# Optimization experiments

Measured on AMD Instinct MI355X. Metric: run time of the kernel, lower is better.

## Reference

```python
import jax, jax.numpy as jnp
import numpy as np


def setup_inputs() -> dict:
    key = jax.random.key(0)
    ks = jax.random.split(key, 7)
    B, H, W, C = 8, 64, 64, 8
    d = C // 8  # q/k/v channels (= 1 here; forced by the module's broadcast-add)
    x = jax.random.normal(ks[0], (B, H, W, C), dtype=jnp.float32)
    # 1x1 convs == per-pixel linear layers: weight (C, d), bias (d,)
    scale = 1.0 / np.sqrt(C)
    Wq = jax.random.normal(ks[1], (C, d), dtype=jnp.float32) * scale
    bq = jnp.zeros((d,), dtype=jnp.float32)
    Wk = jax.random.normal(ks[2], (C, d), dtype=jnp.float32) * scale
    bk = jnp.zeros((d,), dtype=jnp.float32)
    Wv = jax.random.normal(ks[3], (C, d), dtype=jnp.float32) * scale
    bv = jnp.zeros((d,), dtype=jnp.float32)
    gamma = jnp.float32(0.5)  # nonzero so the attention branch matters
    return {"x": x, "Wq": Wq, "bq": bq, "Wk": Wk, "bk": bk, "Wv": Wv, "bv": bv, "gamma": gamma}


def reference(x, Wq, bq, Wk, bk, Wv, bv, gamma):
    B, H, W, C = x.shape
    N = H * W
    # 1x1 conv projections (NHWC, per-pixel linear)
    q = (jnp.einsum('bhwc,cd->bhwd', x, Wq) + bq).reshape(B, N, -1)  # (B,N,d)
    k = (jnp.einsum('bhwc,cd->bhwd', x, Wk) + bk).reshape(B, N, -1)  # (B,N,d)
    v = (jnp.einsum('bhwc,cd->bhwd', x, Wv) + bv).reshape(B, N, -1)  # (B,N,d)
    # energy[b,i,j] = <q_i, k_j>; NOTE: no 1/sqrt(d) scaling, per source
    energy = jnp.einsum('bnd,bmd->bnm', q, k)  # (B,N,N)
    attention = jax.nn.softmax(energy, axis=-1)
    # out[b,i,d] = sum_j attention[b,i,j] * v[b,j,d]
    out = jnp.einsum('bnm,bmd->bnd', attention, v).reshape(B, H, W, -1)  # (B,H,W,d)
    # gamma-scaled residual; d==1 so out broadcasts against C channels
    y = out * gamma + x
    return (y, attention)
```

## Files before the change

### kernel.cpp

```cpp
#include <hip/hip_runtime.h>
#include <math.h>

#define NPIX 4096
#define CCH 8
#define ROWS 32
#define BLK 256
#define NW   (BLK/64)
#define NP   (BLK/ROWS)
#define SEG  (NPIX/NP)
#define L2E 1.44269504088896340736f

typedef float floatx4 __attribute__((ext_vector_type(4)));

__global__ __launch_bounds__(256) void kv_project(
    const float* __restrict__ x,
    const float* __restrict__ Wk, const float* __restrict__ bk,
    const float* __restrict__ Wv, const float* __restrict__ bv,
    float* __restrict__ kbuf, float* __restrict__ vbuf)
{
    const int b = blockIdx.y;
    const int j = blockIdx.x * 256 + threadIdx.x;

    float wk[CCH], wv[CCH];
#pragma unroll
    for (int c = 0; c < CCH; ++c) { wk[c] = Wk[c]; wv[c] = Wv[c]; }
    const float bkv = bk[0], bvv = bv[0];

    const float4* xp = reinterpret_cast<const float4*>(x + ((size_t)b * NPIX + j) * CCH);
    float4 x0 = xp[0];
    float4 x1 = xp[1];
    float kj = bkv;
    kj = fmaf(x0.x, wk[0], kj); kj = fmaf(x0.y, wk[1], kj);
    kj = fmaf(x0.z, wk[2], kj); kj = fmaf(x0.w, wk[3], kj);
    kj = fmaf(x1.x, wk[4], kj); kj = fmaf(x1.y, wk[5], kj);
    kj = fmaf(x1.z, wk[6], kj); kj = fmaf(x1.w, wk[7], kj);
    float vj = bvv;
    vj = fmaf(x0.x, wv[0], vj); vj = fmaf(x0.y, wv[1], vj);
    vj = fmaf(x0.z, wv[2], vj); vj = fmaf(x0.w, wv[3], vj);
    vj = fmaf(x1.x, wv[4], vj); vj = fmaf(x1.y, wv[5], vj);
    vj = fmaf(x1.z, wv[6], vj); vj = fmaf(x1.w, wv[7], vj);

    kbuf[(size_t)b * NPIX + j] = kj;
    vbuf[(size_t)b * NPIX + j] = vj;
}

__global__ __launch_bounds__(BLK) void attn_main(
    const float* __restrict__ x,
    const float* __restrict__ Wq, const float* __restrict__ bq,
    const float* __restrict__ gamma_p,
    const float* __restrict__ kbuf, const float* __restrict__ vbuf,
    float* __restrict__ y, float* __restrict__ attn)
{
    __shared__ float ks[NPIX];
    __shared__ float vs[NPIX];
    __shared__ float qrow[ROWS];
    __shared__ float crow[ROWS];
    __shared__ float spart[NP][ROWS];
    __shared__ float opart[NP][ROWS];
    __shared__ float kred[2][NW];

    const int b = blockIdx.y;
    const int rowbase = blockIdx.x * ROWS;
    const int tid = threadIdx.x;
    const int wid = tid >> 6;
    const int lane = tid & 63;

    float wq[CCH];
#pragma unroll
    for (int c = 0; c < CCH; ++c) wq[c] = Wq[c];
    const float bqv = bq[0];
    const float gamma = gamma_p[0];

    const float* xb = x + (size_t)b * NPIX * CCH;
    const float4* kb4 = reinterpret_cast<const float4*>(kbuf + (size_t)b * NPIX);
    const float4* vb4 = reinterpret_cast<const float4*>(vbuf + (size_t)b * NPIX);

    const int j4 = tid * 4;
    float4 kc[4], vc[4];
    float kmx = -INFINITY, kmn = INFINITY;
#pragma unroll
    for (int g = 0; g < 4; ++g) {
        kc[g] = kb4[tid + g * 256];
        vc[g] = vb4[tid + g * 256];
        *reinterpret_cast<float4*>(&ks[j4 + g * 1024]) = kc[g];
        *reinterpret_cast<float4*>(&vs[j4 + g * 1024]) = vc[g];
        kmx = fmaxf(kmx, fmaxf(fmaxf(kc[g].x, kc[g].y), fmaxf(kc[g].z, kc[g].w)));
        kmn = fminf(kmn, fminf(fminf(kc[g].x, kc[g].y), fminf(kc[g].z, kc[g].w)));
    }
#pragma unroll
    for (int off = 32; off > 0; off >>= 1) {
        kmx = fmaxf(kmx, __shfl_xor(kmx, off));
        kmn = fminf(kmn, __shfl_xor(kmn, off));
    }
    if (lane == 0) { kred[0][wid] = kmx; kred[1][wid] = kmn; }
    __syncthreads();
    kmx = fmaxf(fmaxf(kred[0][0], kred[0][1]), fmaxf(kred[0][2], kred[0][3]));
    kmn = fminf(fminf(kred[1][0], kred[1][1]), fminf(kred[1][2], kred[1][3]));

    const int r = tid & (ROWS - 1);
    const int p = tid >> 5;
    const int i = rowbase + r;
    const float4* xq = reinterpret_cast<const float4*>(xb + (size_t)i * CCH);
    float4 a0 = xq[0];
    float4 a1 = xq[1];
    float q = bqv;
    q = fmaf(a0.x, wq[0], q); q = fmaf(a0.y, wq[1], q);
    q = fmaf(a0.z, wq[2], q); q = fmaf(a0.w, wq[3], q);
    q = fmaf(a1.x, wq[4], q); q = fmaf(a1.y, wq[5], q);
    q = fmaf(a1.z, wq[6], q); q = fmaf(a1.w, wq[7], q);

    const float q2 = q * L2E;
    const float m2 = q2 * ((q >= 0.f) ? kmx : kmn);

    float s0 = 0.f, s1 = 0.f, s2 = 0.f, s3 = 0.f;
    float o0 = 0.f, o1 = 0.f, o2 = 0.f, o3 = 0.f;
    const int j0 = p * SEG;
    for (int j = j0; j < j0 + SEG; j += 4) {
        float4 kk = *reinterpret_cast<const float4*>(&ks[j]);
        float4 vv = *reinterpret_cast<const float4*>(&vs[j]);
        float e0 = exp2f(fmaf(q2, kk.x, -m2));
        float e1 = exp2f(fmaf(q2, kk.y, -m2));
        float e2 = exp2f(fmaf(q2, kk.z, -m2));
        float e3 = exp2f(fmaf(q2, kk.w, -m2));
        s0 += e0; s1 += e1; s2 += e2; s3 += e3;
        o0 = fmaf(e0, vv.x, o0);
        o1 = fmaf(e1, vv.y, o1);
        o2 = fmaf(e2, vv.z, o2);
        o3 = fmaf(e3, vv.w, o3);
    }
    spart[p][r] = (s0 + s1) + (s2 + s3);
    opart[p][r] = (o0 + o1) + (o2 + o3);
    __syncthreads();

    if (tid < ROWS) {
        float s = 0.f, o = 0.f;
#pragma unroll
        for (int pp = 0; pp < NP; ++pp) { s += spart[pp][tid]; o += opart[pp][tid]; }
        const float og = (o / s) * gamma;
        const int i2 = rowbase + tid;
        const float4* xr = reinterpret_cast<const float4*>(xb + (size_t)i2 * CCH);
        float4 b0 = xr[0];
        float4 b1 = xr[1];
        float* yp = y + ((size_t)b * NPIX + i2) * CCH;
        float4 y0 = { og + b0.x, og + b0.y, og + b0.z, og + b0.w };
        float4 y1 = { og + b1.x, og + b1.y, og + b1.z, og + b1.w };
        *reinterpret_cast<float4*>(yp) = y0;
        *reinterpret_cast<float4*>(yp + 4) = y1;
        qrow[tid] = q2;
        crow[tid] = m2 + log2f(s);
    }
    __syncthreads();

    float* ap0 = attn + ((size_t)b * NPIX + rowbase) * (size_t)NPIX + j4;
    for (int rr = 0; rr < ROWS; ++rr) {
        const float qr = qrow[rr];
        const float cr = crow[rr];
        float* ap = ap0 + (size_t)rr * NPIX;
#pragma unroll
        for (int g = 0; g < 4; ++g) {
            floatx4 e;
            e.x = exp2f(fmaf(qr, kc[g].x, -cr));
            e.y = exp2f(fmaf(qr, kc[g].y, -cr));
            e.z = exp2f(fmaf(qr, kc[g].z, -cr));
            e.w = exp2f(fmaf(qr, kc[g].w, -cr));
            __builtin_nontemporal_store(e, reinterpret_cast<floatx4*>(ap + g * 1024));
        }
    }
}

__global__ __launch_bounds__(BLK) void attn_fused(
    const float* __restrict__ x,
    const float* __restrict__ Wq, const float* __restrict__ bq,
    const float* __restrict__ Wk, const float* __restrict__ bk,
    const float* __restrict__ Wv, const float* __restrict__ bv,
    const float* __restrict__ gamma_p,
    float* __restrict__ y, float* __restrict__ attn)
{
    __shared__ float ks[NPIX];
    __shared__ float vs[NPIX];
    __shared__ float qrow[ROWS];
    __shared__ float crow[ROWS];
    __shared__ float spart[NP][ROWS];
    __shared__ float opart[NP][ROWS];
    __shared__ float kred[2][NW];

    const int b = blockIdx.y;
    const int rowbase = blockIdx.x * ROWS;
    const int tid = threadIdx.x;
    const int wid = tid >> 6;
    const int lane = tid & 63;

    float wq[CCH], wk[CCH], wv[CCH];
#pragma unroll
    for (int c = 0; c < CCH; ++c) { wq[c] = Wq[c]; wk[c] = Wk[c]; wv[c] = Wv[c]; }
    const float bqv = bq[0], bkv = bk[0], bvv = bv[0];
    const float gamma = gamma_p[0];
    const float* xb = x + (size_t)b * NPIX * CCH;

    float kmx = -INFINITY, kmn = INFINITY;
    for (int j = tid; j < NPIX; j += BLK) {
        const float4* xp = reinterpret_cast<const float4*>(xb + (size_t)j * CCH);
        float4 x0 = xp[0];
        float4 x1 = xp[1];
        float kj = bkv;
        kj = fmaf(x0.x, wk[0], kj); kj = fmaf(x0.y, wk[1], kj);
        kj = fmaf(x0.z, wk[2], kj); kj = fmaf(x0.w, wk[3], kj);
        kj = fmaf(x1.x, wk[4], kj); kj = fmaf(x1.y, wk[5], kj);
        kj = fmaf(x1.z, wk[6], kj); kj = fmaf(x1.w, wk[7], kj);
        float vj = bvv;
        vj = fmaf(x0.x, wv[0], vj); vj = fmaf(x0.y, wv[1], vj);
        vj = fmaf(x0.z, wv[2], vj); vj = fmaf(x0.w, wv[3], vj);
        vj = fmaf(x1.x, wv[4], vj); vj = fmaf(x1.y, wv[5], vj);
        vj = fmaf(x1.z, wv[6], vj); vj = fmaf(x1.w, wv[7], vj);
        ks[j] = kj; vs[j] = vj;
        kmx = fmaxf(kmx, kj); kmn = fminf(kmn, kj);
    }
#pragma unroll
    for (int off = 32; off > 0; off >>= 1) {
        kmx = fmaxf(kmx, __shfl_xor(kmx, off));
        kmn = fminf(kmn, __shfl_xor(kmn, off));
    }
    if (lane == 0) { kred[0][wid] = kmx; kred[1][wid] = kmn; }
    __syncthreads();
    kmx = fmaxf(fmaxf(kred[0][0], kred[0][1]), fmaxf(kred[0][2], kred[0][3]));
    kmn = fminf(fminf(kred[1][0], kred[1][1]), fminf(kred[1][2], kred[1][3]));

    const int r = tid & (ROWS - 1);
    const int p = tid >> 5;
    const int i = rowbase + r;
    const float4* xq = reinterpret_cast<const float4*>(xb + (size_t)i * CCH);
    float4 a0 = xq[0];
    float4 a1 = xq[1];
    float q = bqv;
    q = fmaf(a0.x, wq[0], q); q = fmaf(a0.y, wq[1], q);
    q = fmaf(a0.z, wq[2], q); q = fmaf(a0.w, wq[3], q);
    q = fmaf(a1.x, wq[4], q); q = fmaf(a1.y, wq[5], q);
    q = fmaf(a1.z, wq[6], q); q = fmaf(a1.w, wq[7], q);
    const float q2 = q * L2E;
    const float m2 = q2 * ((q >= 0.f) ? kmx : kmn);

    float s0 = 0.f, s1 = 0.f, s2 = 0.f, s3 = 0.f;
    float o0 = 0.f, o1 = 0.f, o2 = 0.f, o3 = 0.f;
    const int j0 = p * SEG;
    for (int j = j0; j < j0 + SEG; j += 4) {
        float4 kk = *reinterpret_cast<const float4*>(&ks[j]);
        float4 vv = *reinterpret_cast<const float4*>(&vs[j]);
        float e0 = exp2f(fmaf(q2, kk.x, -m2));
        float e1 = exp2f(fmaf(q2, kk.y, -m2));
        float e2 = exp2f(fmaf(q2, kk.z, -m2));
        float e3 = exp2f(fmaf(q2, kk.w, -m2));
        s0 += e0; s1 += e1; s2 += e2; s3 += e3;
        o0 = fmaf(e0, vv.x, o0);
        o1 = fmaf(e1, vv.y, o1);
        o2 = fmaf(e2, vv.z, o2);
        o3 = fmaf(e3, vv.w, o3);
    }
    spart[p][r] = (s0 + s1) + (s2 + s3);
    opart[p][r] = (o0 + o1) + (o2 + o3);
    __syncthreads();

    if (tid < ROWS) {
        float s = 0.f, o = 0.f;
#pragma unroll
        for (int pp = 0; pp < NP; ++pp) { s += spart[pp][tid]; o += opart[pp][tid]; }
        const float og = (o / s) * gamma;
        const int i2 = rowbase + tid;
        const float4* xr = reinterpret_cast<const float4*>(xb + (size_t)i2 * CCH);
        float4 b0 = xr[0];
        float4 b1 = xr[1];
        float* yp = y + ((size_t)b * NPIX + i2) * CCH;
        float4 y0 = { og + b0.x, og + b0.y, og + b0.z, og + b0.w };
        float4 y1 = { og + b1.x, og + b1.y, og + b1.z, og + b1.w };
        *reinterpret_cast<float4*>(yp) = y0;
        *reinterpret_cast<float4*>(yp + 4) = y1;
        qrow[tid] = q2;
        crow[tid] = m2 + log2f(s);
    }
    __syncthreads();

    const int j4 = tid * 4;
    float4 kk0 = *reinterpret_cast<const float4*>(&ks[j4]);
    float4 kk1 = *reinterpret_cast<const float4*>(&ks[j4 + 1024]);
    float4 kk2 = *reinterpret_cast<const float4*>(&ks[j4 + 2048]);
    float4 kk3 = *reinterpret_cast<const float4*>(&ks[j4 + 3072]);

    float* ap0 = attn + ((size_t)b * NPIX + rowbase) * (size_t)NPIX;
    for (int rr = 0; rr < ROWS; ++rr) {
        const float qr = qrow[rr];
        const float cr = crow[rr];
        float* ap = ap0 + (size_t)rr * NPIX;
        floatx4 e0, e1, e2, e3;
        e0.x = exp2f(fmaf(qr, kk0.x, -cr)); e0.y = exp2f(fmaf(qr, kk0.y, -cr));
        e0.z = exp2f(fmaf(qr, kk0.z, -cr)); e0.w = exp2f(fmaf(qr, kk0.w, -cr));
        e1.x = exp2f(fmaf(qr, kk1.x, -cr)); e1.y = exp2f(fmaf(qr, kk1.y, -cr));
        e1.z = exp2f(fmaf(qr, kk1.z, -cr)); e1.w = exp2f(fmaf(qr, kk1.w, -cr));
        e2.x = exp2f(fmaf(qr, kk2.x, -cr)); e2.y = exp2f(fmaf(qr, kk2.y, -cr));
        e2.z = exp2f(fmaf(qr, kk2.z, -cr)); e2.w = exp2f(fmaf(qr, kk2.w, -cr));
        e3.x = exp2f(fmaf(qr, kk3.x, -cr)); e3.y = exp2f(fmaf(qr, kk3.y, -cr));
        e3.z = exp2f(fmaf(qr, kk3.z, -cr)); e3.w = exp2f(fmaf(qr, kk3.w, -cr));
        __builtin_nontemporal_store(e0, reinterpret_cast<floatx4*>(&ap[j4]));
        __builtin_nontemporal_store(e1, reinterpret_cast<floatx4*>(&ap[j4 + 1024]));
        __builtin_nontemporal_store(e2, reinterpret_cast<floatx4*>(&ap[j4 + 2048]));
        __builtin_nontemporal_store(e3, reinterpret_cast<floatx4*>(&ap[j4 + 3072]));
    }
}

extern "C" void kernel_launch(void* const* d_in, const int* in_sizes, int n_in,
                              void* d_out, int out_size, void* d_ws, size_t ws_size,
                              hipStream_t stream) {
    const float* x   = (const float*)d_in[0];
    const float* Wq  = (const float*)d_in[1];
    const float* bq  = (const float*)d_in[2];
    const float* Wk  = (const float*)d_in[3];
    const float* bk  = (const float*)d_in[4];
    const float* Wv  = (const float*)d_in[5];
    const float* bv  = (const float*)d_in[6];
    const float* gm  = (const float*)d_in[7];

    const int B = in_sizes[0] / (NPIX * CCH);
    float* y    = (float*)d_out;
    float* attn = y + (size_t)B * NPIX * CCH;

    const size_t kv_bytes = (size_t)B * NPIX * 2 * sizeof(float);
    if (ws_size >= kv_bytes) {
        float* kbuf = (float*)d_ws;
        float* vbuf = kbuf + (size_t)B * NPIX;
        dim3 gridA(NPIX / 256, B);
        kv_project<<<gridA, 256, 0, stream>>>(x, Wk, bk, Wv, bv, kbuf, vbuf);
        dim3 gridB(NPIX / ROWS, B);
        attn_main<<<gridB, BLK, 0, stream>>>(x, Wq, bq, gm, kbuf, vbuf, y, attn);
    } else {
        dim3 grid(NPIX / ROWS, B);
        attn_fused<<<grid, BLK, 0, stream>>>(x, Wq, bq, Wk, bk, Wv, bv, gm, y, attn);
    }
}
```

Baseline: 123.4 us.

## Compute each attention row once per wavefront and reuse exps for output

The main kernel previously evaluated every exponential twice: once in a row-partitioned pass to get the softmax sum and weighted value, and again to write the normalized attention matrix. Now each wavefront owns eight query rows. For each row it computes the 4096 exponentials once, keeps them in registers, reduces sum and output with wave shuffles, then writes attention values scaled by the reciprocal sum. This removes half the exp work and the block-level partial-sum syncs. The cost is 64 extra registers for the cached exps, with a launch-bounds occupancy hint added to offset that, plus a slightly different rounding path (multiply by reciprocal instead of subtracting log-sum).

```diff
diff --git a/kernel.cpp b/kernel.cpp
--- a/kernel.cpp
+++ b/kernel.cpp
@@ -3,11 +3,10 @@
 
 #define NPIX 4096
 #define CCH 8
-#define ROWS 32
 #define BLK 256
 #define NW   (BLK/64)
-#define NP   (BLK/ROWS)
-#define SEG  (NPIX/NP)
+#define RPW  8
+#define TILE (NW*RPW)
 #define L2E 1.44269504088896340736f
 
 typedef float floatx4 __attribute__((ext_vector_type(4)));
@@ -44,7 +43,7 @@
     vbuf[(size_t)b * NPIX + j] = vj;
 }
 
-__global__ __launch_bounds__(BLK) void attn_main(
+__global__ __launch_bounds__(BLK, 4) void attn_main(
     const float* __restrict__ x,
     const float* __restrict__ Wq, const float* __restrict__ bq,
     const float* __restrict__ gamma_p,
@@ -53,14 +52,10 @@
 {
     __shared__ float ks[NPIX];
     __shared__ float vs[NPIX];
-    __shared__ float qrow[ROWS];
-    __shared__ float crow[ROWS];
-    __shared__ float spart[NP][ROWS];
-    __shared__ float opart[NP][ROWS];
     __shared__ float kred[2][NW];
 
     const int b = blockIdx.y;
-    const int rowbase = blockIdx.x * ROWS;
+    const int rowbase = blockIdx.x * TILE;
     const int tid = threadIdx.x;
     const int wid = tid >> 6;
     const int lane = tid & 63;
@@ -75,17 +70,16 @@
     const float4* kb4 = reinterpret_cast<const float4*>(kbuf + (size_t)b * NPIX);
     const float4* vb4 = reinterpret_cast<const float4*>(vbuf + (size_t)b * NPIX);
 
-    const int j4 = tid * 4;
-    float4 kc[4], vc[4];
     float kmx = -INFINITY, kmn = INFINITY;
 #pragma unroll
-    for (int g = 0; g < 4; ++g) {
-        kc[g] = kb4[tid + g * 256];
-        vc[g] = vb4[tid + g * 256];
-        *reinterpret_cast<float4*>(&ks[j4 + g * 1024]) = kc[g];
-        *reinterpret_cast<float4*>(&vs[j4 + g * 1024]) = vc[g];
-        kmx = fmaxf(kmx, fmaxf(fmaxf(kc[g].x, kc[g].y), fmaxf(kc[g].z, kc[g].w)));
-        kmn = fminf(kmn, fminf(fminf(kc[g].x, kc[g].y), fminf(kc[g].z, kc[g].w)));
+    for (int i = 0; i < 4; ++i) {
+        const int idx = tid + i * 256;
+        float4 kk = kb4[idx];
+        float4 vv = vb4[idx];
+        *reinterpret_cast<float4*>(&ks[idx * 4]) = kk;
+        *reinterpret_cast<float4*>(&vs[idx * 4]) = vv;
+        kmx = fmaxf(kmx, fmaxf(fmaxf(kk.x, kk.y), fmaxf(kk.z, kk.w)));
+        kmn = fminf(kmn, fminf(fminf(kk.x, kk.y), fminf(kk.z, kk.w)));
     }
 #pragma unroll
     for (int off = 32; off > 0; off >>= 1) {
@@ -97,10 +91,11 @@
     kmx = fmaxf(fmaxf(kred[0][0], kred[0][1]), fmaxf(kred[0][2], kred[0][3]));
     kmn = fminf(fminf(kred[1][0], kred[1][1]), fminf(kred[1][2], kred[1][3]));
 
-    const int r = tid & (ROWS - 1);
-    const int p = tid >> 5;
-    const int i = rowbase + r;
-    const float4* xq = reinterpret_cast<const float4*>(xb + (size_t)i * CCH);
+    const int r8 = lane & 7;
+    const int irow0 = rowbase + wid * RPW;
+    {
+    }
+    const float4* xq = reinterpret_cast<const float4*>(xb + (size_t)(irow0 + r8) * CCH);
     float4 a0 = xq[0];
     float4 a1 = xq[1];
     float q = bqv;
@@ -108,65 +103,62 @@
     q = fmaf(a0.z, wq[2], q); q = fmaf(a0.w, wq[3], q);
     q = fmaf(a1.x, wq[4], q); q = fmaf(a1.y, wq[5], q);
     q = fmaf(a1.z, wq[6], q); q = fmaf(a1.w, wq[7], q);
-
-    const float q2 = q * L2E;
-    const float m2 = q2 * ((q >= 0.f) ? kmx : kmn);
-
-    float s0 = 0.f, s1 = 0.f, s2 = 0.f, s3 = 0.f;
-    float o0 = 0.f, o1 = 0.f, o2 = 0.f, o3 = 0.f;
-    const int j0 = p * SEG;
-    for (int j = j0; j < j0 + SEG; j += 4) {
-        float4 kk = *reinterpret_cast<const float4*>(&ks[j]);
-        float4 vv = *reinterpret_cast<const float4*>(&vs[j]);
-        float e0 = exp2f(fmaf(q2, kk.x, -m2));
-        float e1 = exp2f(fmaf(q2, kk.y, -m2));
-        float e2 = exp2f(fmaf(q2, kk.z, -m2));
-        float e3 = exp2f(fmaf(q2, kk.w, -m2));
-        s0 += e0; s1 += e1; s2 += e2; s3 += e3;
-        o0 = fmaf(e0, vv.x, o0);
-        o1 = fmaf(e1, vv.y, o1);
-        o2 = fmaf(e2, vv.z, o2);
-        o3 = fmaf(e3, vv.w, o3);
-    }
-    spart[p][r] = (s0 + s1) + (s2 + s3);
-    opart[p][r] = (o0 + o1) + (o2 + o3);
-    __syncthreads();
-
-    if (tid < ROWS) {
+    const float q2v = q * L2E;
+    const float m2v = q2v * ((q >= 0.f) ? kmx : kmn);
+
+    const float4* ks4 = reinterpret_cast<const float4*>(ks);
+    const float4* vs4 = reinterpret_cast<const float4*>(vs);
+    float* ap_base = attn + ((size_t)b * NPIX + irow0) * (size_t)NPIX;
+
+    for (int rr = 0; rr < RPW; ++rr) {
+        const float q2r = __shfl(q2v, rr);
+        const float m2r = __shfl(m2v, rr);
+
+        float4 earr[16];
         float s = 0.f, o = 0.f;
 #pragma unroll
-        for (int pp = 0; pp < NP; ++pp) { s += spart[pp][tid]; o += opart[pp][tid]; }
-        const float og = (o / s) * gamma;
-        const int i2 = rowbase + tid;
-        const float4* xr = reinterpret_cast<const float4*>(xb + (size_t)i2 * CCH);
-        float4 b0 = xr[0];
-        float4 b1 = xr[1];
-        float* yp = y + ((size_t)b * NPIX + i2) * CCH;
-        float4 y0 = { og + b0.x, og + b0.y, og + b0.z, og + b0.w };
-        float4 y1 = { og + b1.x, og + b1.y, og + b1.z, og + b1.w };
-        *reinterpret_cast<float4*>(yp) = y0;
-        *reinterpret_cast<float4*>(yp + 4) = y1;
-        qrow[tid] = q2;
-        crow[tid] = m2 + log2f(s);
-    }
-    __syncthreads();
-
-    float* ap0 = attn + ((size_t)b * NPIX + rowbase) * (size_t)NPIX + j4;
-    for (int rr = 0; rr < ROWS; ++rr) {
-        const float qr = qrow[rr];
-        const float cr = crow[rr];
-        float* ap = ap0 + (size_t)rr * NPIX;
-#pragma unroll
-        for (int g = 0; g < 4; ++g) {
+        for (int g = 0; g < 16; ++g) {
+            float4 kk = ks4[lane + g * 64];
+            float4 vv = vs4[lane + g * 64];
+            float e0 = exp2f(fmaf(q2r, kk.x, -m2r));
+            float e1 = exp2f(fmaf(q2r, kk.y, -m2r));
+            float e2 = exp2f(fmaf(q2r, kk.z, -m2r));
+            float e3 = exp2f(fmaf(q2r, kk.w, -m2r));
+            earr[g].x = e0; earr[g].y = e1; earr[g].z = e2; earr[g].w = e3;
+            s += (e0 + e1) + (e2 + e3);
+            o += fmaf(e0, vv.x, e1 * vv.y) + fmaf(e2, vv.z, e3 * vv.w);
+        }
+#pragma unroll
+        for (int off = 32; off > 0; off >>= 1) {
+            s += __shfl_xor(s, off);
+            o += __shfl_xor(o, off);
+        }
+        const float invs = 1.0f / s;
+
+        const int i = irow0 + rr;
+        if (lane < 2) {
+            const float og = o * invs * gamma;
+            const float4 xv = *reinterpret_cast<const float4*>(xb + (size_t)i * CCH + lane * 4);
+            float4 yv = { og + xv.x, og + xv.y, og + xv.z, og + xv.w };
+            *reinterpret_cast<float4*>(y + ((size_t)b * NPIX + i) * CCH + lane * 4) = yv;
+        }
+
+        float* ap = ap_base + (size_t)rr * NPIX;
+#pragma unroll
+        for (int g = 0; g < 16; ++g) {
             floatx4 e;
-            e.x = exp2f(fmaf(qr, kc[g].x, -cr));
-            e.y = exp2f(fmaf(qr, kc[g].y, -cr));
-            e.z = exp2f(fmaf(qr, kc[g].z, -cr));
-            e.w = exp2f(fmaf(qr, kc[g].w, -cr));
-            __builtin_nontemporal_store(e, reinterpret_cast<floatx4*>(ap + g * 1024));
+            e.x = earr[g].x * invs;
+            e.y = earr[g].y * invs;
+            e.z = earr[g].z * invs;
+            e.w = earr[g].w * invs;
+            __builtin_nontemporal_store(e, reinterpret_cast<floatx4*>(ap + lane * 4 + g * 256));
         }
     }
 }
+
+#define ROWS 32
+#define NP   (BLK/ROWS)
+#define SEG  (NPIX/NP)
 
 __global__ __launch_bounds__(BLK) void attn_fused(
     const float* __restrict__ x,
@@ -327,7 +319,7 @@
         float* vbuf = kbuf + (size_t)B * NPIX;
         dim3 gridA(NPIX / 256, B);
         kv_project<<<gridA, 256, 0, stream>>>(x, Wk, bk, Wv, bv, kbuf, vbuf);
-        dim3 gridB(NPIX / ROWS, B);
+        dim3 gridB(NPIX / TILE, B);
         attn_main<<<gridB, BLK, 0, stream>>>(x, Wq, bq, gm, kbuf, vbuf, y, attn);
     } else {
         dim3 grid(NPIX / ROWS, B);
```

Measured after the change: 216.3 us. +75.3%, slower.
